# Kernel optimization log

Measured on AMD Instinct MI355X. Metric: run time of the kernel, lower is better.

## Reference

```python
import jax, jax.numpy as jnp
import numpy as np

N_NODES = 100000
N_EDGES = 1600000
D = 128
N_CLASS = 10
N_LAYERS = 3
BN_EPS = 1e-5


def setup_inputs() -> dict:
    key = jax.random.key(0)
    ks = jax.random.split(key, 12)
    s = 1.0 / np.sqrt(D)
    x = jax.random.normal(ks[0], (N_NODES, D), dtype=jnp.float32)
    edge_index = jax.random.randint(ks[1], (2, N_EDGES), 0, N_NODES, dtype=jnp.int64)
    return {
        "x": x,
        "edge_index": edge_index,
        "W1": jax.random.normal(ks[2], (N_LAYERS, D, D), dtype=jnp.float32) * s,
        "b1": jnp.zeros((N_LAYERS, D), dtype=jnp.float32),
        "gamma": jnp.ones((N_LAYERS, D), dtype=jnp.float32),
        "beta": jnp.zeros((N_LAYERS, D), dtype=jnp.float32),
        "W2": jax.random.normal(ks[3], (N_LAYERS, D, D), dtype=jnp.float32) * s,
        "b2": jnp.zeros((N_LAYERS, D), dtype=jnp.float32),
        "lin1_W": jax.random.normal(ks[4], (D, D), dtype=jnp.float32) * s,
        "lin1_b": jnp.zeros((D,), dtype=jnp.float32),
        "lin2_W": jax.random.normal(ks[5], (N_CLASS, D), dtype=jnp.float32) * s,
        "lin2_b": jnp.zeros((N_CLASS,), dtype=jnp.float32),
    }


def _gin_layer(h, src, dst, W1, b1, g, bt, W2, b2):
    # GINConv with eps=0: mlp((1+eps)*x + sum_{j->i} x_j)
    agg = jax.ops.segment_sum(h[src], dst, num_segments=N_NODES)  # [N, D]
    z = (h + agg) @ W1.T + b1
    # BatchNorm1d (training-mode batch statistics, biased variance)
    mu = jnp.mean(z, axis=0)
    var = jnp.var(z, axis=0)
    z = (z - mu) * jax.lax.rsqrt(var + BN_EPS) * g + bt
    z = jax.nn.relu(z)
    z = jax.nn.relu(z @ W2.T + b2)
    return z


def reference(x, edge_index, W1, b1, gamma, beta, W2, b2, lin1_W, lin1_b, lin2_W, lin2_b):
    src, dst = edge_index[0], edge_index[1]
    h = x.astype(jnp.float32)
    for i in range(N_LAYERS):
        h = _gin_layer(h, src, dst, W1[i], b1[i], gamma[i], beta[i], W2[i], b2[i])
    h = jax.nn.relu(h @ lin1_W.T + lin1_b)
    h = h @ lin2_W.T + lin2_b
    return jax.nn.sigmoid(h)
```

## Files before the change

### kernel.cpp

```cpp
#include <hip/hip_runtime.h>
#include <math.h>

#define N_NODES 100000
#define N_EDGES 1600000
#define D 128
#define NCLASS 10
#define NLAYERS 3
#define BN_EPS 1e-5f

#define LDA 136
#define BUCKET_SH 7
#define NBUK 782
#define NBLK 256
#define CHUNK 6250
#define SCAN_BLKS NBUK

typedef __attribute__((ext_vector_type(8))) short bf16x8;
typedef __attribute__((ext_vector_type(4))) float f32x4;

__device__ __forceinline__ ushort f2b(float x) {
    uint u = __float_as_uint(x);
    return (ushort)((u + 0x7fffu + ((u >> 16) & 1u)) >> 16);
}
__device__ __forceinline__ float b2f(uint u) {
    return __uint_as_float(u << 16);
}
__device__ __forceinline__ uint pack2(float a, float b) {
    return (uint)f2b(a) | ((uint)f2b(b) << 16);
}

__global__ __launch_bounds__(256) void k_hist(const int* __restrict__ dst,
                                              int* __restrict__ hist) {
    __shared__ int lh[NBUK];
    int t = threadIdx.x, b = blockIdx.x;
    for (int i = t; i < NBUK; i += 256) lh[i] = 0;
    __syncthreads();
    int e0 = b * CHUNK;
    for (int e = e0 + t; e < e0 + CHUNK; e += 256)
        atomicAdd(&lh[dst[e] >> BUCKET_SH], 1);
    __syncthreads();
    for (int i = t; i < NBUK; i += 256) hist[i * NBLK + b] = lh[i];
}

__global__ __launch_bounds__(256) void k_scan1(int* __restrict__ hist, int* __restrict__ psums) {
    __shared__ int sh[256];
    int t = threadIdx.x;
    int i = blockIdx.x * 256 + t;
    int v = hist[i];
    sh[t] = v; __syncthreads();
    for (int off = 1; off < 256; off <<= 1) {
        int a = (t >= off) ? sh[t - off] : 0;
        __syncthreads();
        sh[t] += a;
        __syncthreads();
    }
    hist[i] = sh[t] - v;
    if (t == 255) psums[blockIdx.x] = sh[255];
}

__global__ __launch_bounds__(1024) void k_scan2(int* __restrict__ psums) {
    __shared__ int sh[1024];
    int t = threadIdx.x;
    int v = (t < SCAN_BLKS) ? psums[t] : 0;
    sh[t] = v; __syncthreads();
    for (int off = 1; off < 1024; off <<= 1) {
        int a = (t >= off) ? sh[t - off] : 0;
        __syncthreads();
        sh[t] += a;
        __syncthreads();
    }
    if (t < SCAN_BLKS) psums[t] = sh[t] - v;
}

__global__ __launch_bounds__(256) void k_partition(const int* __restrict__ src,
                                                   const int* __restrict__ dst,
                                                   const int* __restrict__ hist,
                                                   const int* __restrict__ psums,
                                                   uint* __restrict__ tmp) {
    __shared__ int lcur[NBUK];
    int t = threadIdx.x, b = blockIdx.x;
    for (int i = t; i < NBUK; i += 256) lcur[i] = hist[i * NBLK + b] + psums[i];
    __syncthreads();
    int e0 = b * CHUNK;
    for (int e = e0 + t; e < e0 + CHUNK; e += 256) {
        int d = dst[e];
        int bk = d >> BUCKET_SH;
        int pos = atomicAdd(&lcur[bk], 1);
        tmp[pos] = (uint)src[e] | ((uint)(d & ((1 << BUCKET_SH) - 1)) << 17);
    }
}

__global__ __launch_bounds__(256) void k_bucket_fill(const uint* __restrict__ tmp,
                                                     const int* __restrict__ psums,
                                                     int* __restrict__ row_ptr,
                                                     int* __restrict__ csr) {
    __shared__ int hist[128], inc[128], cur[128];
    int b = blockIdx.x, t = threadIdx.x;
    int base = psums[b];
    int end  = (b + 1 < NBUK) ? psums[b + 1] : N_EDGES;
    int nb = end - base;
    int lo = b << BUCKET_SH;
    const uint* bt = tmp + base;

    if (t < 128) hist[t] = 0;
    __syncthreads();
    for (int i = t; i < nb; i += 256)
        atomicAdd(&hist[bt[i] >> 17], 1);
    __syncthreads();
    if (t < 128) inc[t] = hist[t];
    __syncthreads();
    for (int offs = 1; offs < 128; offs <<= 1) {
        int a = (t < 128 && t >= offs) ? inc[t - offs] : 0;
        __syncthreads();
        if (t < 128) inc[t] += a;
        __syncthreads();
    }
    if (t < 128) {
        int node = lo + t;
        if (node < N_NODES) row_ptr[node] = base + inc[t] - hist[t];
        cur[t] = 0;
    }
    if (b == NBUK - 1 && t == 0) row_ptr[N_NODES] = base + nb;
    __syncthreads();
    for (int i = t; i < nb; i += 256) {
        uint u = bt[i];
        int dl = u >> 17;
        int s = (int)(u & 0x1ffffu);
        int p = atomicAdd(&cur[dl], 1);
        csr[base + (inc[dl] - hist[dl]) + p] = s;
    }
}

__global__ void k_tobf16(const float* __restrict__ x, ushort* __restrict__ o) {
    int i = blockIdx.x * 256 + threadIdx.x;
    const int n4 = N_NODES * D / 4;
    if (i < n4) {
        float4 v = ((const float4*)x)[i];
        uint2 u;
        u.x = pack2(v.x, v.y);
        u.y = pack2(v.z, v.w);
        ((uint2*)o)[i] = u;
    }
}

__global__ __launch_bounds__(256) void k_aggregate(const ushort* __restrict__ hbf,
                                                   const int* __restrict__ row_ptr,
                                                   const int* __restrict__ csr,
                                                   ushort* __restrict__ outbf) {
    int node = blockIdx.x * 4 + (threadIdx.x >> 6);
    int lane = threadIdx.x & 63;
    const uint* hp = (const uint*)hbf;
    uint self = hp[(size_t)node * 64 + lane];
    float ax = b2f(self & 0xffffu), ay = b2f(self >> 16);
    int e0 = row_ptr[node], e1 = row_ptr[node + 1];
    int e = e0;
    for (; e + 7 < e1; e += 8) {
        uint v0 = hp[(size_t)csr[e]     * 64 + lane];
        uint v1 = hp[(size_t)csr[e + 1] * 64 + lane];
        uint v2 = hp[(size_t)csr[e + 2] * 64 + lane];
        uint v3 = hp[(size_t)csr[e + 3] * 64 + lane];
        uint v4 = hp[(size_t)csr[e + 4] * 64 + lane];
        uint v5 = hp[(size_t)csr[e + 5] * 64 + lane];
        uint v6 = hp[(size_t)csr[e + 6] * 64 + lane];
        uint v7 = hp[(size_t)csr[e + 7] * 64 + lane];
        ax += b2f(v0 & 0xffffu); ay += b2f(v0 >> 16);
        ax += b2f(v1 & 0xffffu); ay += b2f(v1 >> 16);
        ax += b2f(v2 & 0xffffu); ay += b2f(v2 >> 16);
        ax += b2f(v3 & 0xffffu); ay += b2f(v3 >> 16);
        ax += b2f(v4 & 0xffffu); ay += b2f(v4 >> 16);
        ax += b2f(v5 & 0xffffu); ay += b2f(v5 >> 16);
        ax += b2f(v6 & 0xffffu); ay += b2f(v6 >> 16);
        ax += b2f(v7 & 0xffffu); ay += b2f(v7 >> 16);
    }
    for (; e < e1; ++e) {
        uint v = hp[(size_t)csr[e] * 64 + lane];
        ax += b2f(v & 0xffffu); ay += b2f(v >> 16);
    }
    __builtin_nontemporal_store(pack2(ax, ay), (uint*)outbf + (size_t)node * 64 + lane);
}

template <int PRE, int POST, int STATS>
__global__ __launch_bounds__(256, 2) void k_gemm(const ushort* __restrict__ inA,
                                                 const float* __restrict__ W,
                                                 const float* __restrict__ bias,
                                                 const float* __restrict__ scale,
                                                 const float* __restrict__ shift,
                                                 ushort* __restrict__ outp,
                                                 float* __restrict__ gsum,
                                                 float* __restrict__ gsq,
                                                 int nrows) {
    __shared__ ushort sA[128 * LDA];
    __shared__ ushort sB[128 * LDA];
    __shared__ float sbias[128];
    __shared__ float lsum[128], lsq[128];

    int t = threadIdx.x;
    int r0 = blockIdx.x * 128;

    for (int idx = t; idx < 128 * 32; idx += 256) {
        int f = idx >> 5, c4 = (idx & 31) << 2;
        float4 v = *(const float4*)(W + f * 128 + c4);
        ushort4 u;
        u.x = f2b(v.x); u.y = f2b(v.y); u.z = f2b(v.z); u.w = f2b(v.w);
        *(ushort4*)&sB[f * LDA + c4] = u;
    }
    if (t < 128) {
        sbias[t] = bias[t];
        lsum[t] = 0.f; lsq[t] = 0.f;
    }

    for (int idx = t; idx < 128 * 16; idx += 256) {
        int r = idx >> 4, c8 = (idx & 15) << 3;
        int rr = r0 + r;
        uint4 v = make_uint4(0u, 0u, 0u, 0u);
        if (rr < nrows) v = *(const uint4*)(inA + (size_t)rr * 128 + c8);
        if (PRE == 2) {
            float f0 = b2f(v.x & 0xffffu), f1 = b2f(v.x >> 16);
            float f2 = b2f(v.y & 0xffffu), f3 = b2f(v.y >> 16);
            float f4 = b2f(v.z & 0xffffu), f5 = b2f(v.z >> 16);
            float f6 = b2f(v.w & 0xffffu), f7 = b2f(v.w >> 16);
            float4 sc0 = *(const float4*)(scale + c8);
            float4 sc1 = *(const float4*)(scale + c8 + 4);
            float4 sf0 = *(const float4*)(shift + c8);
            float4 sf1 = *(const float4*)(shift + c8 + 4);
            f0 = fmaxf(fmaf(f0, sc0.x, sf0.x), 0.f);
            f1 = fmaxf(fmaf(f1, sc0.y, sf0.y), 0.f);
            f2 = fmaxf(fmaf(f2, sc0.z, sf0.z), 0.f);
            f3 = fmaxf(fmaf(f3, sc0.w, sf0.w), 0.f);
            f4 = fmaxf(fmaf(f4, sc1.x, sf1.x), 0.f);
            f5 = fmaxf(fmaf(f5, sc1.y, sf1.y), 0.f);
            f6 = fmaxf(fmaf(f6, sc1.z, sf1.z), 0.f);
            f7 = fmaxf(fmaf(f7, sc1.w, sf1.w), 0.f);
            v.x = pack2(f0, f1); v.y = pack2(f2, f3);
            v.z = pack2(f4, f5); v.w = pack2(f6, f7);
        }
        *(uint4*)&sA[r * LDA + c8] = v;
    }
    __syncthreads();

    int lane = t & 63, wid = t >> 6;
    int rl = lane & 15, g = lane >> 4;
    int wr = wid >> 1, wc = wid & 1;

    f32x4 acc[4][4];
#pragma unroll
    for (int i = 0; i < 4; ++i)
#pragma unroll
        for (int j = 0; j < 4; ++j) acc[i][j] = (f32x4){0.f, 0.f, 0.f, 0.f};

#pragma unroll
    for (int ks = 0; ks < 4; ++ks) {
        int koff = ks * 32 + g * 8;
        bf16x8 a[4], b[4];
#pragma unroll
        for (int mi = 0; mi < 4; ++mi)
            a[mi] = *(const bf16x8*)&sA[(wr * 64 + mi * 16 + rl) * LDA + koff];
#pragma unroll
        for (int ni = 0; ni < 4; ++ni)
            b[ni] = *(const bf16x8*)&sB[(wc * 64 + ni * 16 + rl) * LDA + koff];
#pragma unroll
        for (int mi = 0; mi < 4; ++mi)
#pragma unroll
            for (int ni = 0; ni < 4; ++ni)
                acc[mi][ni] = __builtin_amdgcn_mfma_f32_16x16x32_bf16(a[mi], b[ni], acc[mi][ni], 0, 0, 0);
    }

    float bn[4], ssum[4], ssq[4];
#pragma unroll
    for (int ni = 0; ni < 4; ++ni) {
        bn[ni] = sbias[wc * 64 + ni * 16 + rl];
        ssum[ni] = 0.f; ssq[ni] = 0.f;
    }

#pragma unroll
    for (int mi = 0; mi < 4; ++mi) {
        int orow = r0 + wr * 64 + mi * 16 + g * 4;
#pragma unroll
        for (int j = 0; j < 4; ++j) {
            int row = orow + j;
            if (row < nrows) {
#pragma unroll
                for (int ni = 0; ni < 4; ++ni) {
                    int ocol = wc * 64 + ni * 16 + rl;
                    float o = acc[mi][ni][j] + bn[ni];
                    if (STATS) { ssum[ni] += o; ssq[ni] += o * o; }
                    if (POST) o = fmaxf(o, 0.f);
                    outp[(size_t)row * 128 + ocol] = f2b(o);
                }
            }
        }
    }

    if (STATS) {
#pragma unroll
        for (int ni = 0; ni < 4; ++ni) {
            float s = ssum[ni], q = ssq[ni];
            s += __shfl_xor(s, 16, 64); q += __shfl_xor(q, 16, 64);
            s += __shfl_xor(s, 32, 64); q += __shfl_xor(q, 32, 64);
            if (g == 0) {
                int col = wc * 64 + ni * 16 + rl;
                atomicAdd(&lsum[col], s);
                atomicAdd(&lsq[col], q);
            }
        }
        __syncthreads();
        if (t < 128) {
            atomicAdd(&gsum[t], lsum[t]);
            atomicAdd(&gsq[t], lsq[t]);
        }
    }
}

__global__ void k_bnfin(float* __restrict__ gsum, float* __restrict__ gsq,
                        const float* __restrict__ gamma, const float* __restrict__ beta,
                        float* __restrict__ scale, float* __restrict__ shift) {
    int d = threadIdx.x;
    float s = gsum[d], q = gsq[d];
    float mu = s * (1.f / N_NODES);
    float var = q * (1.f / N_NODES) - mu * mu;
    float rstd = rsqrtf(var + BN_EPS);
    float sc = rstd * gamma[d];
    scale[d] = sc;
    shift[d] = beta[d] - mu * sc;
    gsum[d] = 0.f;
    gsq[d] = 0.f;
}

__global__ __launch_bounds__(256, 2) void k_head(const ushort* __restrict__ hbf,
                                                 const float* __restrict__ W1,
                                                 const float* __restrict__ b1f,
                                                 const float* __restrict__ W2,
                                                 const float* __restrict__ b2f_,
                                                 float* __restrict__ out) {
    __shared__ ushort sA[128 * LDA];
    __shared__ ushort sB[128 * LDA];
    __shared__ float sbias[128];
    __shared__ float w2s[NCLASS * 128];
    __shared__ float b2s[NCLASS];

    int t = threadIdx.x;
    int r0 = blockIdx.x * 128;

    for (int idx = t; idx < 128 * 32; idx += 256) {
        int f = idx >> 5, c4 = (idx & 31) << 2;
        float4 v = *(const float4*)(W1 + f * 128 + c4);
        ushort4 u;
        u.x = f2b(v.x); u.y = f2b(v.y); u.z = f2b(v.z); u.w = f2b(v.w);
        *(ushort4*)&sB[f * LDA + c4] = u;
    }
    if (t < 128) sbias[t] = b1f[t];
    for (int idx = t; idx < (NCLASS * 128) / 4; idx += 256)
        *(float4*)&w2s[idx * 4] = *(const float4*)(W2 + idx * 4);
    if (t < NCLASS) b2s[t] = b2f_[t];

    for (int idx = t; idx < 128 * 16; idx += 256) {
        int r = idx >> 4, c8 = (idx & 15) << 3;
        int rr = r0 + r;
        uint4 v = make_uint4(0u, 0u, 0u, 0u);
        if (rr < N_NODES) v = *(const uint4*)(hbf + (size_t)rr * 128 + c8);
        *(uint4*)&sA[r * LDA + c8] = v;
    }
    __syncthreads();

    int lane = t & 63, wid = t >> 6;
    int rl = lane & 15, g = lane >> 4;
    int wr = wid >> 1, wc = wid & 1;

    f32x4 acc[4][4];
#pragma unroll
    for (int i = 0; i < 4; ++i)
#pragma unroll
        for (int j = 0; j < 4; ++j) acc[i][j] = (f32x4){0.f, 0.f, 0.f, 0.f};

#pragma unroll
    for (int ks = 0; ks < 4; ++ks) {
        int koff = ks * 32 + g * 8;
        bf16x8 a[4], b[4];
#pragma unroll
        for (int mi = 0; mi < 4; ++mi)
            a[mi] = *(const bf16x8*)&sA[(wr * 64 + mi * 16 + rl) * LDA + koff];
#pragma unroll
        for (int ni = 0; ni < 4; ++ni)
            b[ni] = *(const bf16x8*)&sB[(wc * 64 + ni * 16 + rl) * LDA + koff];
#pragma unroll
        for (int mi = 0; mi < 4; ++mi)
#pragma unroll
            for (int ni = 0; ni < 4; ++ni)
                acc[mi][ni] = __builtin_amdgcn_mfma_f32_16x16x32_bf16(a[mi], b[ni], acc[mi][ni], 0, 0, 0);
    }

    __syncthreads();

    float bn[4];
#pragma unroll
    for (int ni = 0; ni < 4; ++ni) bn[ni] = sbias[wc * 64 + ni * 16 + rl];
#pragma unroll
    for (int mi = 0; mi < 4; ++mi) {
        int rowl = wr * 64 + mi * 16 + g * 4;
#pragma unroll
        for (int j = 0; j < 4; ++j) {
#pragma unroll
            for (int ni = 0; ni < 4; ++ni) {
                int ocol = wc * 64 + ni * 16 + rl;
                float o = fmaxf(acc[mi][ni][j] + bn[ni], 0.f);
                sA[ocol * LDA + rowl + j] = f2b(o);
            }
        }
    }
    __syncthreads();

    int row = t & 127, ch = t >> 7;
    float acc2[5] = {0.f, 0.f, 0.f, 0.f, 0.f};
    const float* w2p = &w2s[ch * 5 * 128];
#pragma unroll 4
    for (int k = 0; k < 128; ++k) {
        float v = b2f(sA[k * LDA + row]);
#pragma unroll
        for (int c = 0; c < 5; ++c)
            acc2[c] = fmaf(v, w2p[c * 128 + k], acc2[c]);
    }
    int rr = r0 + row;
    if (rr < N_NODES) {
#pragma unroll
        for (int c = 0; c < 5; ++c) {
            float z = acc2[c] + b2s[ch * 5 + c];
            out[(size_t)rr * NCLASS + ch * 5 + c] = 1.f / (1.f + expf(-z));
        }
    }
}

extern "C" void kernel_launch(void* const* d_in, const int* in_sizes, int n_in,
                              void* d_out, int out_size, void* d_ws, size_t ws_size,
                              hipStream_t stream) {
    const float* x     = (const float*)d_in[0];
    const int*   ei    = (const int*)d_in[1];
    const float* W1    = (const float*)d_in[2];
    const float* b1    = (const float*)d_in[3];
    const float* gamma = (const float*)d_in[4];
    const float* beta  = (const float*)d_in[5];
    const float* W2    = (const float*)d_in[6];
    const float* b2    = (const float*)d_in[7];
    const float* l1W   = (const float*)d_in[8];
    const float* l1b   = (const float*)d_in[9];
    const float* l2W   = (const float*)d_in[10];
    const float* l2b   = (const float*)d_in[11];
    float* out = (float*)d_out;

    char* w = (char*)d_ws;
    ushort* hbf    = (ushort*)(w);
    ushort* zbf    = (ushort*)(w + 25600000);
    ushort* aggout = (ushort*)(w + 51200000);
    int*   row_ptr = (int*)   (w + 76800000);
    int*   csr     = (int*)   (w + 77200640);
    uint*  tmp     = (uint*)  (w + 83600640);
    int*   hist    = (int*)   (w + 90000640);
    int*   psums   = (int*)   (w + 90801920);
    float* gsum    = (float*) (w + 90806016);
    float* gsq     = gsum + 128;
    float* scale   = gsum + 256;
    float* shift   = gsum + 384;

    const int* src = ei;
    const int* dst = ei + N_EDGES;

    const int GEMM_NB = (N_NODES + 127) / 128;

    hipMemsetAsync(gsum, 0, 256 * sizeof(float), stream);

    k_hist<<<NBLK, 256, 0, stream>>>(dst, hist);
    k_scan1<<<SCAN_BLKS, 256, 0, stream>>>(hist, psums);
    k_scan2<<<1, 1024, 0, stream>>>(psums);
    k_partition<<<NBLK, 256, 0, stream>>>(src, dst, hist, psums, tmp);
    k_bucket_fill<<<NBUK, 256, 0, stream>>>(tmp, psums, row_ptr, csr);

    k_tobf16<<<(N_NODES * D / 4 + 255) / 256, 256, 0, stream>>>(x, hbf);

    for (int l = 0; l < NLAYERS; ++l) {
        k_aggregate<<<N_NODES / 4, 256, 0, stream>>>(hbf, row_ptr, csr, aggout);
        k_gemm<0, 0, 1><<<GEMM_NB, 256, 0, stream>>>(aggout, W1 + l * D * D, b1 + l * D,
                                                     nullptr, nullptr, zbf, gsum, gsq, N_NODES);
        k_bnfin<<<1, 128, 0, stream>>>(gsum, gsq, gamma + l * D, beta + l * D, scale, shift);
        k_gemm<2, 1, 0><<<GEMM_NB, 256, 0, stream>>>(zbf, W2 + l * D * D, b2 + l * D,
                                                     scale, shift, hbf, nullptr, nullptr, N_NODES);
    }

    k_head<<<GEMM_NB, 256, 0, stream>>>(hbf, l1W, l1b, l2W, l2b, out);
}
```

Baseline: 497.3 us.

## Preconvert weights to bf16 once, read B from global, and split-edge aggregation

All weight matrices are converted to bf16 once, inside the fused input-conversion kernel. The GEMM and head kernels then drop their shared-memory B tile and read B fragments straight from global/L2, which halves LDS use and raises launch_bounds occupancy. The aggregation kernel now has each wave half process alternate edges with 8-byte loads and combines the halves with a cross-lane shuffle. Streaming inputs use nontemporal loads. The trade-off is repeated global reads of the weights per wave, and nontemporal loads on gathered neighbour rows could hurt L2 reuse.

```diff
diff --git a/kernel.cpp b/kernel.cpp
--- a/kernel.cpp
+++ b/kernel.cpp
@@ -17,6 +17,8 @@
 
 typedef __attribute__((ext_vector_type(8))) short bf16x8;
 typedef __attribute__((ext_vector_type(4))) float f32x4;
+typedef __attribute__((ext_vector_type(2))) uint u32x2;
+typedef __attribute__((ext_vector_type(4))) uint u32x4;
 
 __device__ __forceinline__ ushort f2b(float x) {
     uint u = __float_as_uint(x);
@@ -131,15 +133,29 @@
     }
 }
 
-__global__ void k_tobf16(const float* __restrict__ x, ushort* __restrict__ o) {
+__global__ void k_conv(const float* __restrict__ x, const float* __restrict__ W1,
+                       const float* __restrict__ W2, const float* __restrict__ l1W,
+                       ushort* __restrict__ hbf, ushort* __restrict__ wbf) {
     int i = blockIdx.x * 256 + threadIdx.x;
-    const int n4 = N_NODES * D / 4;
-    if (i < n4) {
+    const int n4x = N_NODES * D / 4;
+    if (i < n4x) {
         float4 v = ((const float4*)x)[i];
-        uint2 u;
+        u32x2 u;
         u.x = pack2(v.x, v.y);
         u.y = pack2(v.z, v.w);
-        ((uint2*)o)[i] = u;
+        ((u32x2*)hbf)[i] = u;
+    } else {
+        int k = i - n4x;
+        const float* srcp;
+        ushort* dstp;
+        if (k < 12288)      { srcp = W1 + k * 4;            dstp = wbf + k * 4; }
+        else if (k < 24576) { srcp = W2 + (k - 12288) * 4;  dstp = wbf + 49152 + (k - 12288) * 4; }
+        else if (k < 28672) { srcp = l1W + (k - 24576) * 4; dstp = wbf + 98304 + (k - 24576) * 4; }
+        else return;
+        float4 v = *(const float4*)srcp;
+        ushort4 u;
+        u.x = f2b(v.x); u.y = f2b(v.y); u.z = f2b(v.z); u.w = f2b(v.w);
+        *(ushort4*)dstp = u;
     }
 }
 
@@ -149,39 +165,58 @@
                                                    ushort* __restrict__ outbf) {
     int node = blockIdx.x * 4 + (threadIdx.x >> 6);
     int lane = threadIdx.x & 63;
-    const uint* hp = (const uint*)hbf;
-    uint self = hp[(size_t)node * 64 + lane];
-    float ax = b2f(self & 0xffffu), ay = b2f(self >> 16);
+    int sub = lane >> 5;
+    int c = lane & 31;
+    const u32x2* hp = (const u32x2*)hbf;
+    u32x2 sv = hp[(size_t)node * 32 + c];
+    float a0 = 0.f, a1 = 0.f, a2 = 0.f, a3 = 0.f;
     int e0 = row_ptr[node], e1 = row_ptr[node + 1];
     int e = e0;
-    for (; e + 7 < e1; e += 8) {
-        uint v0 = hp[(size_t)csr[e]     * 64 + lane];
-        uint v1 = hp[(size_t)csr[e + 1] * 64 + lane];
-        uint v2 = hp[(size_t)csr[e + 2] * 64 + lane];
-        uint v3 = hp[(size_t)csr[e + 3] * 64 + lane];
-        uint v4 = hp[(size_t)csr[e + 4] * 64 + lane];
-        uint v5 = hp[(size_t)csr[e + 5] * 64 + lane];
-        uint v6 = hp[(size_t)csr[e + 6] * 64 + lane];
-        uint v7 = hp[(size_t)csr[e + 7] * 64 + lane];
-        ax += b2f(v0 & 0xffffu); ay += b2f(v0 >> 16);
-        ax += b2f(v1 & 0xffffu); ay += b2f(v1 >> 16);
-        ax += b2f(v2 & 0xffffu); ay += b2f(v2 >> 16);
-        ax += b2f(v3 & 0xffffu); ay += b2f(v3 >> 16);
-        ax += b2f(v4 & 0xffffu); ay += b2f(v4 >> 16);
-        ax += b2f(v5 & 0xffffu); ay += b2f(v5 >> 16);
-        ax += b2f(v6 & 0xffffu); ay += b2f(v6 >> 16);
-        ax += b2f(v7 & 0xffffu); ay += b2f(v7 >> 16);
-    }
-    for (; e < e1; ++e) {
-        uint v = hp[(size_t)csr[e] * 64 + lane];
-        ax += b2f(v & 0xffffu); ay += b2f(v >> 16);
-    }
-    __builtin_nontemporal_store(pack2(ax, ay), (uint*)outbf + (size_t)node * 64 + lane);
+    for (; e + 15 < e1; e += 16) {
+        u32x2 v0 = __builtin_nontemporal_load(&hp[(size_t)csr[e      + sub] * 32 + c]);
+        u32x2 v1 = __builtin_nontemporal_load(&hp[(size_t)csr[e + 2  + sub] * 32 + c]);
+        u32x2 v2 = __builtin_nontemporal_load(&hp[(size_t)csr[e + 4  + sub] * 32 + c]);
+        u32x2 v3 = __builtin_nontemporal_load(&hp[(size_t)csr[e + 6  + sub] * 32 + c]);
+        u32x2 v4 = __builtin_nontemporal_load(&hp[(size_t)csr[e + 8  + sub] * 32 + c]);
+        u32x2 v5 = __builtin_nontemporal_load(&hp[(size_t)csr[e + 10 + sub] * 32 + c]);
+        u32x2 v6 = __builtin_nontemporal_load(&hp[(size_t)csr[e + 12 + sub] * 32 + c]);
+        u32x2 v7 = __builtin_nontemporal_load(&hp[(size_t)csr[e + 14 + sub] * 32 + c]);
+        a0 += b2f(v0.x & 0xffffu); a1 += b2f(v0.x >> 16); a2 += b2f(v0.y & 0xffffu); a3 += b2f(v0.y >> 16);
+        a0 += b2f(v1.x & 0xffffu); a1 += b2f(v1.x >> 16); a2 += b2f(v1.y & 0xffffu); a3 += b2f(v1.y >> 16);
+        a0 += b2f(v2.x & 0xffffu); a1 += b2f(v2.x >> 16); a2 += b2f(v2.y & 0xffffu); a3 += b2f(v2.y >> 16);
+        a0 += b2f(v3.x & 0xffffu); a1 += b2f(v3.x >> 16); a2 += b2f(v3.y & 0xffffu); a3 += b2f(v3.y >> 16);
+        a0 += b2f(v4.x & 0xffffu); a1 += b2f(v4.x >> 16); a2 += b2f(v4.y & 0xffffu); a3 += b2f(v4.y >> 16);
+        a0 += b2f(v5.x & 0xffffu); a1 += b2f(v5.x >> 16); a2 += b2f(v5.y & 0xffffu); a3 += b2f(v5.y >> 16);
+        a0 += b2f(v6.x & 0xffffu); a1 += b2f(v6.x >> 16); a2 += b2f(v6.y & 0xffffu); a3 += b2f(v6.y >> 16);
+        a0 += b2f(v7.x & 0xffffu); a1 += b2f(v7.x >> 16); a2 += b2f(v7.y & 0xffffu); a3 += b2f(v7.y >> 16);
+    }
+    for (; e + 1 < e1; e += 2) {
+        u32x2 v = __builtin_nontemporal_load(&hp[(size_t)csr[e + sub] * 32 + c]);
+        a0 += b2f(v.x & 0xffffu); a1 += b2f(v.x >> 16);
+        a2 += b2f(v.y & 0xffffu); a3 += b2f(v.y >> 16);
+    }
+    if (e < e1 && sub == 0) {
+        u32x2 v = __builtin_nontemporal_load(&hp[(size_t)csr[e] * 32 + c]);
+        a0 += b2f(v.x & 0xffffu); a1 += b2f(v.x >> 16);
+        a2 += b2f(v.y & 0xffffu); a3 += b2f(v.y >> 16);
+    }
+    a0 += __shfl_xor(a0, 32, 64);
+    a1 += __shfl_xor(a1, 32, 64);
+    a2 += __shfl_xor(a2, 32, 64);
+    a3 += __shfl_xor(a3, 32, 64);
+    a0 += b2f(sv.x & 0xffffu); a1 += b2f(sv.x >> 16);
+    a2 += b2f(sv.y & 0xffffu); a3 += b2f(sv.y >> 16);
+    if (sub == 0) {
+        u32x2 o;
+        o.x = pack2(a0, a1);
+        o.y = pack2(a2, a3);
+        __builtin_nontemporal_store(o, (u32x2*)outbf + (size_t)node * 32 + c);
+    }
 }
 
 template <int PRE, int POST, int STATS>
-__global__ __launch_bounds__(256, 2) void k_gemm(const ushort* __restrict__ inA,
-                                                 const float* __restrict__ W,
+__global__ __launch_bounds__(256, 4) void k_gemm(const ushort* __restrict__ inA,
+                                                 const ushort* __restrict__ Wbf,
                                                  const float* __restrict__ bias,
                                                  const float* __restrict__ scale,
                                                  const float* __restrict__ shift,
@@ -190,20 +225,12 @@
                                                  float* __restrict__ gsq,
                                                  int nrows) {
     __shared__ ushort sA[128 * LDA];
-    __shared__ ushort sB[128 * LDA];
     __shared__ float sbias[128];
     __shared__ float lsum[128], lsq[128];
 
     int t = threadIdx.x;
     int r0 = blockIdx.x * 128;
 
-    for (int idx = t; idx < 128 * 32; idx += 256) {
-        int f = idx >> 5, c4 = (idx & 31) << 2;
-        float4 v = *(const float4*)(W + f * 128 + c4);
-        ushort4 u;
-        u.x = f2b(v.x); u.y = f2b(v.y); u.z = f2b(v.z); u.w = f2b(v.w);
-        *(ushort4*)&sB[f * LDA + c4] = u;
-    }
     if (t < 128) {
         sbias[t] = bias[t];
         lsum[t] = 0.f; lsq[t] = 0.f;
@@ -212,8 +239,8 @@
     for (int idx = t; idx < 128 * 16; idx += 256) {
         int r = idx >> 4, c8 = (idx & 15) << 3;
         int rr = r0 + r;
-        uint4 v = make_uint4(0u, 0u, 0u, 0u);
-        if (rr < nrows) v = *(const uint4*)(inA + (size_t)rr * 128 + c8);
+        u32x4 v = (u32x4){0u, 0u, 0u, 0u};
+        if (rr < nrows) v = __builtin_nontemporal_load((const u32x4*)(inA + (size_t)rr * 128 + c8));
         if (PRE == 2) {
             float f0 = b2f(v.x & 0xffffu), f1 = b2f(v.x >> 16);
             float f2 = b2f(v.y & 0xffffu), f3 = b2f(v.y >> 16);
@@ -234,7 +261,7 @@
             v.x = pack2(f0, f1); v.y = pack2(f2, f3);
             v.z = pack2(f4, f5); v.w = pack2(f6, f7);
         }
-        *(uint4*)&sA[r * LDA + c8] = v;
+        *(u32x4*)&sA[r * LDA + c8] = v;
     }
     __syncthreads();
 
@@ -253,11 +280,11 @@
         int koff = ks * 32 + g * 8;
         bf16x8 a[4], b[4];
 #pragma unroll
+        for (int ni = 0; ni < 4; ++ni)
+            b[ni] = *(const bf16x8*)&Wbf[(size_t)(wc * 64 + ni * 16 + rl) * 128 + koff];
+#pragma unroll
         for (int mi = 0; mi < 4; ++mi)
             a[mi] = *(const bf16x8*)&sA[(wr * 64 + mi * 16 + rl) * LDA + koff];
-#pragma unroll
-        for (int ni = 0; ni < 4; ++ni)
-            b[ni] = *(const bf16x8*)&sB[(wc * 64 + ni * 16 + rl) * LDA + koff];
 #pragma unroll
         for (int mi = 0; mi < 4; ++mi)
 #pragma unroll
@@ -326,14 +353,13 @@
     gsq[d] = 0.f;
 }
 
-__global__ __launch_bounds__(256, 2) void k_head(const ushort* __restrict__ hbf,
-                                                 const float* __restrict__ W1,
+__global__ __launch_bounds__(256, 3) void k_head(const ushort* __restrict__ hbf,
+                                                 const ushort* __restrict__ l1bf,
                                                  const float* __restrict__ b1f,
                                                  const float* __restrict__ W2,
                                                  const float* __restrict__ b2f_,
                                                  float* __restrict__ out) {
     __shared__ ushort sA[128 * LDA];
-    __shared__ ushort sB[128 * LDA];
     __shared__ float sbias[128];
     __shared__ float w2s[NCLASS * 128];
     __shared__ float b2s[NCLASS];
@@ -341,13 +367,6 @@
     int t = threadIdx.x;
     int r0 = blockIdx.x * 128;
 
-    for (int idx = t; idx < 128 * 32; idx += 256) {
-        int f = idx >> 5, c4 = (idx & 31) << 2;
-        float4 v = *(const float4*)(W1 + f * 128 + c4);
-        ushort4 u;
-        u.x = f2b(v.x); u.y = f2b(v.y); u.z = f2b(v.z); u.w = f2b(v.w);
-        *(ushort4*)&sB[f * LDA + c4] = u;
-    }
     if (t < 128) sbias[t] = b1f[t];
     for (int idx = t; idx < (NCLASS * 128) / 4; idx += 256)
         *(float4*)&w2s[idx * 4] = *(const float4*)(W2 + idx * 4);
@@ -356,9 +375,9 @@
     for (int idx = t; idx < 128 * 16; idx += 256) {
         int r = idx >> 4, c8 = (idx & 15) << 3;
         int rr = r0 + r;
-        uint4 v = make_uint4(0u, 0u, 0u, 0u);
-        if (rr < N_NODES) v = *(const uint4*)(hbf + (size_t)rr * 128 + c8);
-        *(uint4*)&sA[r * LDA + c8] = v;
+        u32x4 v = (u32x4){0u, 0u, 0u, 0u};
+        if (rr < N_NODES) v = __builtin_nontemporal_load((const u32x4*)(hbf + (size_t)rr * 128 + c8));
+        *(u32x4*)&sA[r * LDA + c8] = v;
     }
     __syncthreads();
 
@@ -377,11 +396,11 @@
         int koff = ks * 32 + g * 8;
         bf16x8 a[4], b[4];
 #pragma unroll
+        for (int ni = 0; ni < 4; ++ni)
+            b[ni] = *(const bf16x8*)&l1bf[(size_t)(wc * 64 + ni * 16 + rl) * 128 + koff];
+#pragma unroll
         for (int mi = 0; mi < 4; ++mi)
             a[mi] = *(const bf16x8*)&sA[(wr * 64 + mi * 16 + rl) * LDA + koff];
-#pragma unroll
-        for (int ni = 0; ni < 4; ++ni)
-            b[ni] = *(const bf16x8*)&sB[(wc * 64 + ni * 16 + rl) * LDA + koff];
 #pragma unroll
         for (int mi = 0; mi < 4; ++mi)
 #pragma unroll
@@ -459,13 +478,17 @@
     float* gsq     = gsum + 128;
     float* scale   = gsum + 256;
     float* shift   = gsum + 384;
+    ushort* wbf    = (ushort*)(w + 90808064);
+    ushort* w1bf   = wbf;
+    ushort* w2bf   = wbf + 49152;
+    ushort* l1bf   = wbf + 98304;
 
     const int* src = ei;
     const int* dst = ei + N_EDGES;
 
     const int GEMM_NB = (N_NODES + 127) / 128;
 
-    hipMemsetAsync(gsum, 0, 256 * sizeof(float), stream);
+    (void)hipMemsetAsync(gsum, 0, 256 * sizeof(float), stream);
 
     k_hist<<<NBLK, 256, 0, stream>>>(dst, hist);
     k_scan1<<<SCAN_BLKS, 256, 0, stream>>>(hist, psums);
@@ -473,16 +496,17 @@
     k_partition<<<NBLK, 256, 0, stream>>>(src, dst, hist, psums, tmp);
     k_bucket_fill<<<NBUK, 256, 0, stream>>>(tmp, psums, row_ptr, csr);
 
-    k_tobf16<<<(N_NODES * D / 4 + 255) / 256, 256, 0, stream>>>(x, hbf);
+    const int CONV_NB = (N_NODES * D / 4 + 28672 + 255) / 256;
+    k_conv<<<CONV_NB, 256, 0, stream>>>(x, W1, W2, l1W, hbf, wbf);
 
     for (int l = 0; l < NLAYERS; ++l) {
         k_aggregate<<<N_NODES / 4, 256, 0, stream>>>(hbf, row_ptr, csr, aggout);
-        k_gemm<0, 0, 1><<<GEMM_NB, 256, 0, stream>>>(aggout, W1 + l * D * D, b1 + l * D,
+        k_gemm<0, 0, 1><<<GEMM_NB, 256, 0, stream>>>(aggout, w1bf + l * D * D, b1 + l * D,
                                                      nullptr, nullptr, zbf, gsum, gsq, N_NODES);
         k_bnfin<<<1, 128, 0, stream>>>(gsum, gsq, gamma + l * D, beta + l * D, scale, shift);
-        k_gemm<2, 1, 0><<<GEMM_NB, 256, 0, stream>>>(zbf, W2 + l * D * D, b2 + l * D,
+        k_gemm<2, 1, 0><<<GEMM_NB, 256, 0, stream>>>(zbf, w2bf + l * D * D, b2 + l * D,
                                                      scale, shift, hbf, nullptr, nullptr, N_NODES);
     }
 
-    k_head<<<GEMM_NB, 256, 0, stream>>>(hbf, l1W, l1b, l2W, l2b, out);
-}
+    k_head<<<GEMM_NB, 256, 0, stream>>>(hbf, l1bf, l1b, l2W, l2b, out);
+}
```

New measurement: 580.9 us. +16.8%, slower.
